# Kernel optimization log

Measured on AMD Instinct MI355X. Metric: run time of the kernel, lower is better.

## Reference

```python
import jax, jax.numpy as jnp
import numpy as np

B_, L_, H_ = 2, 2048, 2048          # batch, seq_len, hidden_size
I_, N_, NH, P_ = 4096, 128, 64, 64   # intermediate, ssm_state, num_heads, head_dim
K_, CH = 4, 256                      # conv kernel, chunk size
DT_MIN, DT_MAX = 0.0, 1e10


def setup_inputs() -> dict:
    key = jax.random.key(0)
    ks = jax.random.split(key, 8)
    conv_dim = I_ + 2 * N_
    proj_out = 2 * (I_ + N_) + NH
    return {
        "hidden_states": jax.random.normal(ks[0], (B_, L_, H_), jnp.float32),
        "W_in": jax.random.normal(ks[1], (proj_out, H_), jnp.float32) * 0.02,
        "conv_w": jax.random.normal(ks[2], (conv_dim, 1, K_), jnp.float32) * 0.2,
        "conv_b": jnp.zeros((conv_dim,), jnp.float32),
        "dt_bias": jax.random.uniform(ks[3], (NH,), jnp.float32),
        "A_log": jnp.log(jax.random.uniform(ks[4], (NH,), jnp.float32, 1.0, 16.0)),
        "D": jnp.ones((NH,), jnp.float32),
        "norm_w": jnp.ones((I_,), jnp.float32),
        "W_out": jax.random.normal(ks[5], (H_, I_), jnp.float32) * 0.02,
    }


def _segsum(x):
    # stable segment-sum: out[..., i, j] = sum_{k=j+1..i} x[..., k] for i>=j, else -inf
    T = x.shape[-1]
    xr = jnp.broadcast_to(x[..., None], x.shape + (T,))
    lower = jnp.tril(jnp.ones((T, T), bool), -1)
    s = jnp.cumsum(jnp.where(lower, xr, 0.0), axis=-2)
    return jnp.where(jnp.tril(jnp.ones((T, T), bool)), s, -jnp.inf)


def reference(hidden_states, W_in, conv_w, conv_b, dt_bias, A_log, D, norm_w, W_out):
    b, L, _ = hidden_states.shape
    proj = hidden_states @ W_in.T                       # (b, L, 2*(I+N)+H)
    z, xBC, dt = jnp.split(proj, [I_, 2 * I_ + 2 * N_], axis=-1)

    # depthwise causal conv1d + silu
    x_t = xBC.transpose(0, 2, 1)                        # (b, conv_dim, L)
    conv = jax.lax.conv_general_dilated(
        x_t, conv_w, (1,), [(K_ - 1, 0)],
        dimension_numbers=("NCH", "OIH", "NCH"), feature_group_count=I_ + 2 * N_)
    xBC = jax.nn.silu((conv + conv_b[None, :, None]).transpose(0, 2, 1))
    x, Bm, Cm = jnp.split(xBC, [I_, I_ + N_], axis=-1)  # (b,L,I) (b,L,N) (b,L,N)

    # ---- SSD naive (chunked state-space-duality scan) ----
    A = -jnp.exp(A_log.astype(jnp.float32))             # (h,)
    dt = jnp.clip(jax.nn.softplus(dt + dt_bias), DT_MIN, DT_MAX)  # (b,L,h)
    x4 = x.reshape(b, L, NH, P_)
    pad = (-L) % CH
    padf = lambda t: jnp.pad(t, [(0, 0), (0, pad)] + [(0, 0)] * (t.ndim - 2))
    D_res = D[None, None, :, None] * padf(x4)           # (b, Lp, h, p)
    xs = padf(x4 * dt[..., None])
    Ah = padf(A[None, None, :] * dt)                    # (b, Lp, h)
    Bc, Cc = padf(Bm), padf(Cm)
    c = (L + pad) // CH
    xs = xs.reshape(b, c, CH, NH, P_)                   # (b,c,l,h,p)
    Ah = Ah.reshape(b, c, CH, NH).transpose(0, 3, 1, 2) # (b,h,c,l)
    Bc = Bc.reshape(b, c, CH, N_)
    Cc = Cc.reshape(b, c, CH, N_)

    A_cs = jnp.cumsum(Ah, axis=-1)                      # (b,h,c,l)
    Lm = jnp.exp(_segsum(Ah))                           # (b,h,c,l,l)
    # intra-chunk (diagonal block) output; B/C shared across heads (n_groups=1)
    Y_diag = jnp.einsum("bcln,bcsn,bhcls,bcshp->bclhp", Cc, Bc, Lm, xs)

    decay_states = jnp.exp(A_cs[..., -1:] - A_cs)       # (b,h,c,l)
    states = jnp.einsum("bcln,bhcl,bclhp->bchpn", Bc, decay_states, xs)
    states = jnp.concatenate([jnp.zeros_like(states[:, :1]), states], axis=1)
    decay_chunk = jnp.exp(_segsum(jnp.pad(A_cs[..., -1], [(0, 0), (0, 0), (1, 0)])))
    new_states = jnp.einsum("bhzc,bchpn->bzhpn", decay_chunk, states)
    states = new_states[:, :-1]                         # (b,c,h,p,n)
    Y_off = jnp.einsum("bcln,bchpn,bhcl->bclhp", Cc, states, jnp.exp(A_cs))

    y = (Y_diag + Y_off).reshape(b, c * CH, NH, P_) + D_res
    y = y[:, :L].reshape(b, L, I_)

    # gated RMSNorm (normalize=True: multiply by silu(residual) before norm)
    yf = y.astype(jnp.float32) * jax.nn.silu(z.astype(jnp.float32))
    yf = yf * jax.lax.rsqrt(jnp.mean(yf * yf, -1, keepdims=True) + 1e-5) * norm_w
    return yf.astype(hidden_states.dtype) @ W_out.T
```

## Files before the change

### kernel.cpp

```cpp
#include <hip/hip_runtime.h>
#include <hip/hip_bf16.h>
#include <math.h>


#define B_SZ 2
#define L_SZ 2048
#define H_SZ 2048
#define I_SZ 4096
#define N_SZ 128
#define NH_SZ 64
#define P_SZ 64
#define CH_SZ 256
#define NC_SZ 8
#define PROJ_SZ 8512
#define CONV_SZ 4352
#define XOFF 4096
#define DTOFF 8448
#define BOFF 4096
#define COFF 4224

typedef __attribute__((ext_vector_type(8))) short short8_t;
typedef __attribute__((ext_vector_type(4))) float float4_t;

#define GLDS(gp, lp)                                                   \
  __builtin_amdgcn_global_load_lds(                                    \
      (const __attribute__((address_space(1))) void*)(gp),             \
      (__attribute__((address_space(3))) void*)(lp), 16, 0, 0)

__device__ __forceinline__ float bf2f(unsigned short u) {
  union { unsigned int i; float f; } v; v.i = ((unsigned int)u) << 16; return v.f;
}
__device__ __forceinline__ unsigned short f2bf(float f) {
  union { float f; unsigned int i; } v; v.f = f;
  unsigned int b = v.i + 0x7fffu + ((v.i >> 16) & 1u);
  return (unsigned short)(b >> 16);
}
__device__ __forceinline__ void unpack8(uint4 v, float* f) {
  f[0] = bf2f((unsigned short)(v.x & 0xffffu)); f[1] = bf2f((unsigned short)(v.x >> 16));
  f[2] = bf2f((unsigned short)(v.y & 0xffffu)); f[3] = bf2f((unsigned short)(v.y >> 16));
  f[4] = bf2f((unsigned short)(v.z & 0xffffu)); f[5] = bf2f((unsigned short)(v.z >> 16));
  f[6] = bf2f((unsigned short)(v.w & 0xffffu)); f[7] = bf2f((unsigned short)(v.w >> 16));
}
__device__ __forceinline__ float silu_f(float x) { return x / (1.f + expf(-x)); }

__device__ __forceinline__ float load1(const void* p, long long e, int fp32) {
  return fp32 ? ((const float*)p)[e] : bf2f(((const unsigned short*)p)[e]);
}
__device__ __forceinline__ void load4(const void* p, long long e, int fp32, float* f) {
  if (fp32) {
    float4 a = *(const float4*)((const float*)p + e);
    f[0] = a.x; f[1] = a.y; f[2] = a.z; f[3] = a.w;
  } else {
    uint2 v = *(const uint2*)((const unsigned short*)p + e);
    f[0] = bf2f((unsigned short)(v.x & 0xffffu)); f[1] = bf2f((unsigned short)(v.x >> 16));
    f[2] = bf2f((unsigned short)(v.y & 0xffffu)); f[3] = bf2f((unsigned short)(v.y >> 16));
  }
}
__device__ __forceinline__ void load8(const void* p, long long e, int fp32, float* f) {
  if (fp32) {
    float4 a = *(const float4*)((const float*)p + e);
    float4 b = *(const float4*)((const float*)p + e + 4);
    f[0] = a.x; f[1] = a.y; f[2] = a.z; f[3] = a.w;
    f[4] = b.x; f[5] = b.y; f[6] = b.z; f[7] = b.w;
  } else {
    uint4 v = *(const uint4*)((const unsigned short*)p + e);
    unpack8(v, f);
  }
}
__device__ __forceinline__ short8_t pack_bf8(const float* p) {
  float4 a = *(const float4*)p;
  float4 b = *(const float4*)(p + 4);
  short8_t r;
  r[0] = (short)f2bf(a.x); r[1] = (short)f2bf(a.y);
  r[2] = (short)f2bf(a.z); r[3] = (short)f2bf(a.w);
  r[4] = (short)f2bf(b.x); r[5] = (short)f2bf(b.y);
  r[6] = (short)f2bf(b.z); r[7] = (short)f2bf(b.w);
  return r;
}

__global__ void detect_k(const void* p0, const void* p1, const void* p2,
                         const void* p3, const void* p4, const void* p5,
                         const void* p6, const void* p7, const void* p8,
                         int n0, int n1, int n2, int n3, int n4, int n5,
                         int n6, int n7, int n8, int* flags) {
  __shared__ int pe, po;
  const void* ps[9] = {p0, p1, p2, p3, p4, p5, p6, p7, p8};
  int ns[9] = {n0, n1, n2, n3, n4, n5, n6, n7, n8};
  int t = threadIdx.x;
  for (int i = 0; i < 9; i++) {
    if (t == 0) { pe = 0; po = 0; }
    __syncthreads();
    int S = ns[i] < 256 ? ns[i] : 256;
    if (t < S) {
      unsigned short u = ((const unsigned short*)ps[i])[t];
      int ex = (u >> 7) & 0xFF;
      int plaus = ((u & 0x7FFFu) != 0) && (ex >= 0x70) && (ex <= 0x8F);
      if (plaus) { if (t & 1) atomicAdd(&po, 1); else atomicAdd(&pe, 1); }
    }
    __syncthreads();
    if (t == 0) flags[i] = (2 * pe < po) ? 1 : 0;
    __syncthreads();
  }
  if (t == 0) { flags[14] = 0; flags[15] = 0; }
}

__global__ __launch_bounds__(256)
void cvt_bf16_k(const void* __restrict__ src, unsigned short* __restrict__ dst,
                long long n8, const int* __restrict__ flags, int fi) {
  long long g = (long long)blockIdx.x * 256 + threadIdx.x;
  if (g >= n8) return;
  long long e = g * 8;
  if (flags[fi]) {
    const float* s = (const float*)src + e;
    float4 a = *(const float4*)s;
    float4 b = *(const float4*)(s + 4);
    unsigned short o[8] = {f2bf(a.x), f2bf(a.y), f2bf(a.z), f2bf(a.w),
                           f2bf(b.x), f2bf(b.y), f2bf(b.z), f2bf(b.w)};
    *(uint4*)(dst + e) = *(const uint4*)o;
  } else {
    *(uint4*)(dst + e) = *(const uint4*)((const unsigned short*)src + e);
  }
}

#define MFMA_ACC(d, a, b) \
  d = __builtin_amdgcn_mfma_f32_16x16x32_bf16(a, b, d, 0, 0, 0)
#define LDA_FR(buf, i, kk) \
  (*(const short8_t*)&As[(buf)*16384 + (wm*128 + (i)*16 + l16)*64 + \
                         (((((kk)<<2) + quad) ^ l7) << 3)])
#define LDB_FR(buf, j, kk) \
  (*(const short8_t*)&Bs[(buf)*16384 + (wn*64 + (j)*16 + l16)*64 + \
                         (((((kk)<<2) + quad) ^ l7) << 3)])
#define STAGE_A(h, tile, buf) do {                                          \
    GLDS(aSrc[h][0] + ((long long)(tile) << 6),                             \
         &As[(buf)*16384 + (h)*8192 + (wave*16)*64]);                       \
    GLDS(aSrc[h][1] + ((long long)(tile) << 6),                             \
         &As[(buf)*16384 + (h)*8192 + (wave*16 + 8)*64]);                   \
  } while (0)
#define STAGE_B(h, tile, buf) do {                                          \
    GLDS(bSrc[h][0] + ((long long)(tile) << 6),                             \
         &Bs[(buf)*16384 + (h)*8192 + (wave*16)*64]);                       \
    GLDS(bSrc[h][1] + ((long long)(tile) << 6),                             \
         &Bs[(buf)*16384 + (h)*8192 + (wave*16 + 8)*64]);                   \
  } while (0)

__global__ __launch_bounds__(512, 2)
void gemm_8ph_k(const unsigned short* __restrict__ A,
                const unsigned short* __restrict__ B,
                unsigned short* __restrict__ C,
                int N, int K, int lda, int ldb, int ldc, int gxTiles) {
  __shared__ alignas(16) unsigned short As[2 * 256 * 64];
  __shared__ alignas(16) unsigned short Bs[2 * 256 * 64];
  const int t = threadIdx.x;
  const int lane = t & 63;
  const int wave = t >> 6;
  const int quad = lane >> 4;
  const int l16 = lane & 15;
  const int l7 = lane & 7;
  const int l3 = lane >> 3;
  const int wm = wave >> 2;
  const int wn = wave & 3;

  int id = blockIdx.x;
  const int nwg = gridDim.x;
  int swz = id;
  if ((nwg & 7) == 0) swz = (id & 7) * (nwg >> 3) + (id >> 3);
  const int band = gxTiles << 2;
  const int by = (swz & 3) + ((swz / band) << 2);
  const int bx = (swz >> 2) % gxTiles;
  const int m0 = by << 8;
  const int n0 = bx << 8;
  const int NT = K >> 6;

  const int kperm = ((l7 ^ l3) << 3);
  const unsigned short* aSrc[2][2];
  const unsigned short* bSrc[2][2];
#pragma unroll
  for (int h = 0; h < 2; ++h)
#pragma unroll
    for (int c = 0; c < 2; ++c) {
      const int rloc = h * 128 + wave * 16 + c * 8 + l3;
      aSrc[h][c] = A + (long long)(m0 + rloc) * lda + kperm;
      int bn = n0 + rloc;
      if (bn > N - 1) bn = N - 1;
      bSrc[h][c] = B + (long long)bn * ldb + kperm;
    }

  float4_t acc[8][4];
#pragma unroll
  for (int i = 0; i < 8; ++i)
#pragma unroll
    for (int j = 0; j < 4; ++j) acc[i][j] = (float4_t){0.f, 0.f, 0.f, 0.f};

  STAGE_A(0, 0, 0); STAGE_A(1, 0, 0);
  STAGE_B(0, 0, 0); STAGE_B(1, 0, 0);
  STAGE_B(0, 1, 1); STAGE_B(1, 1, 1);
  asm volatile("s_waitcnt vmcnt(4)" ::: "memory");
  __builtin_amdgcn_s_barrier();

  short8_t af[4][2], bf[4][2];
  for (int tt = 0; tt < NT; ++tt) {
    const int rb = tt & 1, nb = rb ^ 1;
#pragma unroll
    for (int i = 0; i < 4; ++i) af[i][0] = LDA_FR(rb, i, 0);
#pragma unroll
    for (int j = 0; j < 4; ++j) bf[j][0] = LDB_FR(rb, j, 0);
    if (tt + 1 < NT) STAGE_A(0, tt + 1, nb);
    asm volatile("s_waitcnt lgkmcnt(4)" ::: "memory");
    __builtin_amdgcn_s_barrier();
    asm volatile("s_waitcnt lgkmcnt(0)" ::: "memory");
    __builtin_amdgcn_s_setprio(1);
#pragma unroll
    for (int i = 0; i < 4; ++i)
#pragma unroll
      for (int j = 0; j < 4; ++j) MFMA_ACC(acc[i][j], af[i][0], bf[j][0]);
    __builtin_amdgcn_s_setprio(0);
    __builtin_amdgcn_s_barrier();
#pragma unroll
    for (int i = 0; i < 4; ++i) af[i][1] = LDA_FR(rb, i, 1);
#pragma unroll
    for (int j = 0; j < 4; ++j) bf[j][1] = LDB_FR(rb, j, 1);
    if (tt + 1 < NT) STAGE_A(1, tt + 1, nb);
    asm volatile("s_waitcnt lgkmcnt(4)" ::: "memory");
    __builtin_amdgcn_s_barrier();
    asm volatile("s_waitcnt lgkmcnt(0)" ::: "memory");
    __builtin_amdgcn_s_setprio(1);
#pragma unroll
    for (int i = 0; i < 4; ++i)
#pragma unroll
      for (int j = 0; j < 4; ++j) MFMA_ACC(acc[i][j], af[i][1], bf[j][1]);
    __builtin_amdgcn_s_setprio(0);
    __builtin_amdgcn_s_barrier();
#pragma unroll
    for (int i = 0; i < 4; ++i) af[i][0] = LDA_FR(rb, 4 + i, 0);
    if (tt + 2 < NT) STAGE_B(0, tt + 2, rb);
    __builtin_amdgcn_s_barrier();
    asm volatile("s_waitcnt lgkmcnt(0)" ::: "memory");
    __builtin_amdgcn_s_setprio(1);
#pragma unroll
    for (int i = 0; i < 4; ++i)
#pragma unroll
      for (int j = 0; j < 4; ++j) MFMA_ACC(acc[4 + i][j], af[i][0], bf[j][0]);
    __builtin_amdgcn_s_setprio(0);
    __builtin_amdgcn_s_barrier();
#pragma unroll
    for (int i = 0; i < 4; ++i) af[i][1] = LDA_FR(rb, 4 + i, 1);
    if (tt + 2 < NT) STAGE_B(1, tt + 2, rb);
    __builtin_amdgcn_s_barrier();
    asm volatile("s_waitcnt lgkmcnt(0)" ::: "memory");
    __builtin_amdgcn_s_setprio(1);
#pragma unroll
    for (int i = 0; i < 4; ++i)
#pragma unroll
      for (int j = 0; j < 4; ++j) MFMA_ACC(acc[4 + i][j], af[i][1], bf[j][1]);
    __builtin_amdgcn_s_setprio(0);
    if (tt < NT - 2) asm volatile("s_waitcnt vmcnt(4)" ::: "memory");
    else             asm volatile("s_waitcnt vmcnt(0)" ::: "memory");
    __builtin_amdgcn_s_barrier();
  }

#pragma unroll
  for (int i = 0; i < 8; ++i) {
#pragma unroll
    for (int r = 0; r < 4; ++r) {
      const int m = m0 + wm * 128 + i * 16 + quad * 4 + r;
      const long long cb = (long long)m * ldc;
#pragma unroll
      for (int j = 0; j < 4; ++j) {
        const int n = n0 + wn * 64 + j * 16 + l16;
        if (n < N) C[cb + n] = f2bf(acc[i][j][r]);
      }
    }
  }
}

#define LDA2(buf, i, kk) \
  (*(const short8_t*)&As2[(buf)*8192 + (wm*64 + (i)*16 + l16)*64 + \
                          (((((kk)<<2) + quad) ^ l7) << 3)])
#define LDB2(buf, j, kk) \
  (*(const short8_t*)&Bs2[(buf)*8192 + (wn*64 + (j)*16 + l16)*64 + \
                          (((((kk)<<2) + quad) ^ l7) << 3)])

template <int OUT_MODE>
__global__ __launch_bounds__(256, 2)
void gemm_2ph_k(const unsigned short* __restrict__ A,
                const unsigned short* __restrict__ B,
                void* __restrict__ Cptr,
                int N, int K, int lda, int ldb, int ldc, int gxTiles,
                const int* __restrict__ flags, int fo) {
  __shared__ alignas(16) unsigned short As2[2 * 128 * 64];
  __shared__ alignas(16) unsigned short Bs2[2 * 128 * 64];
  const int t = threadIdx.x;
  const int lane = t & 63;
  const int wave = t >> 6;
  const int quad = lane >> 4;
  const int l16 = lane & 15;
  const int l7 = lane & 7;
  const int l3 = lane >> 3;
  const int wm = wave >> 1;
  const int wn = wave & 1;
  const int ofp = (OUT_MODE == 2) ? flags[fo] : 0;

  int id = blockIdx.x;
  const int nwg = gridDim.x;
  int swz = id;
  if ((nwg & 7) == 0) swz = (id & 7) * (nwg >> 3) + (id >> 3);
  const int band = gxTiles << 2;
  const int by = (swz & 3) + ((swz / band) << 2);
  const int bx = (swz >> 2) % gxTiles;
  const int m0 = by << 7;
  const int n0 = bx << 7;
  const int NT = K >> 6;

  const int kperm = ((l7 ^ l3) << 3);
  const unsigned short* aSrc[4];
  const unsigned short* bSrc[4];
#pragma unroll
  for (int c = 0; c < 4; ++c) {
    aSrc[c] = A + (long long)(m0 + wave * 32 + c * 8 + l3) * lda + kperm;
    int bn = n0 + wave * 32 + c * 8 + l3;
    if (bn > N - 1) bn = N - 1;
    bSrc[c] = B + (long long)bn * ldb + kperm;
  }

  float4_t acc[4][4];
#pragma unroll
  for (int i = 0; i < 4; ++i)
#pragma unroll
    for (int j = 0; j < 4; ++j) acc[i][j] = (float4_t){0.f, 0.f, 0.f, 0.f};

#pragma unroll
  for (int c = 0; c < 4; ++c) {
    GLDS(aSrc[c], &As2[(wave * 32 + c * 8) * 64]);
    GLDS(bSrc[c], &Bs2[(wave * 32 + c * 8) * 64]);
  }
  asm volatile("s_waitcnt vmcnt(0)" ::: "memory");
  __builtin_amdgcn_s_barrier();

  short8_t af[4], bfr[4];
  for (int tt = 0; tt < NT; ++tt) {
    const int rb = tt & 1, nb = rb ^ 1;
#pragma unroll
    for (int i = 0; i < 4; ++i) af[i] = LDA2(rb, i, 0);
#pragma unroll
    for (int j = 0; j < 4; ++j) bfr[j] = LDB2(rb, j, 0);
    if (tt + 1 < NT) {
      const long long ko = (long long)(tt + 1) << 6;
#pragma unroll
      for (int c = 0; c < 4; ++c) {
        GLDS(aSrc[c] + ko, &As2[nb * 8192 + (wave * 32 + c * 8) * 64]);
        GLDS(bSrc[c] + ko, &Bs2[nb * 8192 + (wave * 32 + c * 8) * 64]);
      }
    }
    __builtin_amdgcn_s_setprio(1);
#pragma unroll
    for (int i = 0; i < 4; ++i)
#pragma unroll
      for (int j = 0; j < 4; ++j) MFMA_ACC(acc[i][j], af[i], bfr[j]);
    __builtin_amdgcn_s_setprio(0);
#pragma unroll
    for (int i = 0; i < 4; ++i) af[i] = LDA2(rb, i, 1);
#pragma unroll
    for (int j = 0; j < 4; ++j) bfr[j] = LDB2(rb, j, 1);
    __builtin_amdgcn_s_setprio(1);
#pragma unroll
    for (int i = 0; i < 4; ++i)
#pragma unroll
      for (int j = 0; j < 4; ++j) MFMA_ACC(acc[i][j], af[i], bfr[j]);
    __builtin_amdgcn_s_setprio(0);
    asm volatile("s_waitcnt vmcnt(0)" ::: "memory");
    __builtin_amdgcn_s_barrier();
  }

#pragma unroll
  for (int i = 0; i < 4; ++i) {
#pragma unroll
    for (int r = 0; r < 4; ++r) {
      const int m = m0 + wm * 64 + i * 16 + quad * 4 + r;
      const long long cb = (long long)m * ldc;
#pragma unroll
      for (int j = 0; j < 4; ++j) {
        const int n = n0 + wn * 64 + j * 16 + l16;
        if (n < N) {
          float v = acc[i][j][r];
          if (ofp) ((float*)Cptr)[cb + n] = v;
          else     ((unsigned short*)Cptr)[cb + n] = f2bf(v);
        }
      }
    }
  }
}

__global__ __launch_bounds__(256)
void gemm_g_k(const unsigned short* __restrict__ convx,
              float* __restrict__ Gm) {
  const int t = threadIdx.x;
  const int lane = t & 63;
  const int wave = t >> 6;
  const int quad = lane >> 4;
  const int l16 = lane & 15;
  const int wm = wave >> 1, wn = wave & 1;
  const int m0 = blockIdx.y * 128 + wm * 64;
  const int n0 = blockIdx.x * 128 + wn * 64;
  const long long row0 = (long long)blockIdx.z * 256;

  float4_t acc[4][4];
#pragma unroll
  for (int i = 0; i < 4; ++i)
#pragma unroll
    for (int j = 0; j < 4; ++j) acc[i][j] = (float4_t){0.f, 0.f, 0.f, 0.f};

#pragma unroll
  for (int kt = 0; kt < 4; ++kt) {
    const int ko = kt * 32 + quad * 8;
    short8_t a[4], b[4];
#pragma unroll
    for (int i = 0; i < 4; ++i)
      a[i] = *(const short8_t*)&convx[(row0 + m0 + i * 16 + l16) * CONV_SZ + COFF + ko];
#pragma unroll
    for (int j = 0; j < 4; ++j)
      b[j] = *(const short8_t*)&convx[(row0 + n0 + j * 16 + l16) * CONV_SZ + BOFF + ko];
#pragma unroll
    for (int i = 0; i < 4; ++i)
#pragma unroll
      for (int j = 0; j < 4; ++j) MFMA_ACC(acc[i][j], a[i], b[j]);
  }
  float* Gb = Gm + (long long)blockIdx.z * 65536;
#pragma unroll
  for (int i = 0; i < 4; ++i)
#pragma unroll
    for (int r = 0; r < 4; ++r) {
      const int m = m0 + i * 16 + quad * 4 + r;
#pragma unroll
      for (int j = 0; j < 4; ++j)
        Gb[(long long)m * 256 + n0 + j * 16 + l16] = acc[i][j][r];
    }
}

__global__ __launch_bounds__(256)
void conv_silu_k(const unsigned short* __restrict__ proj,
                 const void* __restrict__ cw,
                 const void* __restrict__ cb,
                 unsigned short* __restrict__ convx,
                 const int* __restrict__ flags) {
  const int total = B_SZ * L_SZ * (CONV_SZ / 4);
  int g = blockIdx.x * 256 + threadIdx.x;
  if (g >= total) return;
  const int fw = flags[2], fb = flags[3];
  int c4 = g % (CONV_SZ / 4);
  int bl = g / (CONV_SZ / 4);
  int l = bl & (L_SZ - 1);
  int ch = c4 * 4;
  float w0[8], w1[8];
  load8(cw, (long long)ch * 4, fw, w0);
  load8(cw, (long long)ch * 4 + 8, fw, w1);
  float accv[4];
  load4(cb, ch, fb, accv);
  float acc0 = accv[0], acc1 = accv[1], acc2 = accv[2], acc3 = accv[3];
  const long long rb = (long long)(bl - l);
#pragma unroll
  for (int k = 0; k < 4; k++) {
    int ls = l - 3 + k;
    if (ls < 0) continue;
    uint2 xv = *(const uint2*)(proj + (rb + ls) * PROJ_SZ + XOFF + ch);
    float x0 = bf2f((unsigned short)(xv.x & 0xffffu));
    float x1 = bf2f((unsigned short)(xv.x >> 16));
    float x2 = bf2f((unsigned short)(xv.y & 0xffffu));
    float x3 = bf2f((unsigned short)(xv.y >> 16));
    acc0 = fmaf(x0, w0[k], acc0);
    acc1 = fmaf(x1, w0[4 + k], acc1);
    acc2 = fmaf(x2, w1[k], acc2);
    acc3 = fmaf(x3, w1[4 + k], acc3);
  }
  unsigned short o0 = f2bf(silu_f(acc0));
  unsigned short o1 = f2bf(silu_f(acc1));
  unsigned short o2 = f2bf(silu_f(acc2));
  unsigned short o3 = f2bf(silu_f(acc3));
  *(uint2*)(convx + (long long)bl * CONV_SZ + ch) =
      make_uint2((unsigned int)o0 | ((unsigned int)o1 << 16),
                 (unsigned int)o2 | ((unsigned int)o3 << 16));
}

__global__ __launch_bounds__(256)
void dt_prep_k(const unsigned short* __restrict__ proj,
               const void* __restrict__ dt_bias,
               float* __restrict__ dtv, const int* __restrict__ flags) {
  int g = blockIdx.x * 256 + threadIdx.x;
  int h = g & 63;
  long long bl = g >> 6;
  float v = bf2f(proj[bl * PROJ_SZ + DTOFF + h]) + load1(dt_bias, h, flags[4]);
  float sp = (v > 20.f) ? v : log1pf(expf(v));
  dtv[g] = sp;
}

__global__ __launch_bounds__(256)
void acs_scan_k(const float* __restrict__ dtv,
                const void* __restrict__ A_log,
                float* __restrict__ acs, const int* __restrict__ flags) {
  __shared__ float sd[256];
  int blk = blockIdx.x;
  int h = blk & 63;
  int bc = blk >> 6;
  int l = threadIdx.x;
  float Ah = -expf(load1(A_log, h, flags[5]));
  long long row = (long long)bc * CH_SZ + l;
  sd[l] = Ah * dtv[row * NH_SZ + h];
  for (int off = 1; off < 256; off <<= 1) {
    __syncthreads();
    float tv = (l >= off) ? sd[l - off] : 0.f;
    __syncthreads();
    sd[l] += tv;
  }
  acs[(long long)blk * CH_SZ + l] = sd[l];
}

__global__ __launch_bounds__(256)
void chunk_states_k(const unsigned short* __restrict__ convx,
                    const float* __restrict__ dtv,
                    const float* __restrict__ acs,
                    float* __restrict__ stc) {
  __shared__ float Bw[32][128];
  __shared__ float xw[32][64];
  int blk = blockIdx.x;
  int h = blk & 63;
  int bc = blk >> 6;
  int t = threadIdx.x;
  const int p0 = (t & 15) * 4, n0 = (t >> 4) * 8;
  const float* acsb = acs + (long long)blk * 256;
  const float alast = acsb[255];
  float acc[4][8];
#pragma unroll
  for (int i = 0; i < 4; i++)
#pragma unroll
    for (int j = 0; j < 8; j++) acc[i][j] = 0.f;
  const long long row0 = (long long)bc * 256;

  for (int lt0 = 0; lt0 < 256; lt0 += 32) {
    __syncthreads();
#pragma unroll
    for (int q = 0; q < 4; q++) {
      int idx4 = (t + 256 * q) * 4;
      int r = idx4 >> 7, n = idx4 & 127;
      uint2 v = *(const uint2*)(convx + (row0 + lt0 + r) * CONV_SZ + BOFF + n);
      Bw[r][n]     = bf2f((unsigned short)(v.x & 0xffffu));
      Bw[r][n + 1] = bf2f((unsigned short)(v.x >> 16));
      Bw[r][n + 2] = bf2f((unsigned short)(v.y & 0xffffu));
      Bw[r][n + 3] = bf2f((unsigned short)(v.y >> 16));
    }
#pragma unroll
    for (int q = 0; q < 2; q++) {
      int idx4 = (t + 256 * q) * 4;
      int r = idx4 >> 6, p = idx4 & 63;
      long long lg = row0 + lt0 + r;
      float sc = dtv[lg * NH_SZ + h] * expf(alast - acsb[lt0 + r]);
      uint2 v = *(const uint2*)(convx + lg * CONV_SZ + h * 64 + p);
      xw[r][p]     = bf2f((unsigned short)(v.x & 0xffffu)) * sc;
      xw[r][p + 1] = bf2f((unsigned short)(v.x >> 16)) * sc;
      xw[r][p + 2] = bf2f((unsigned short)(v.y & 0xffffu)) * sc;
      xw[r][p + 3] = bf2f((unsigned short)(v.y >> 16)) * sc;
    }
    __syncthreads();
#pragma unroll 4
    for (int lt = 0; lt < 32; lt++) {
      float4 xv = *(const float4*)&xw[lt][p0];
      float4 b0 = *(const float4*)&Bw[lt][n0];
      float4 b1 = *(const float4*)&Bw[lt][n0 + 4];
      float xa[4] = {xv.x, xv.y, xv.z, xv.w};
      float ba[8] = {b0.x, b0.y, b0.z, b0.w, b1.x, b1.y, b1.z, b1.w};
#pragma unroll
      for (int i = 0; i < 4; i++)
#pragma unroll
        for (int j = 0; j < 8; j++) acc[i][j] = fmaf(xa[i], ba[j], acc[i][j]);
    }
  }
  float* outb = stc + (long long)blk * 8192;
#pragma unroll
  for (int i = 0; i < 4; i++) {
    *(float4*)&outb[(p0 + i) * 128 + n0] =
        make_float4(acc[i][0], acc[i][1], acc[i][2], acc[i][3]);
    *(float4*)&outb[(p0 + i) * 128 + n0 + 4] =
        make_float4(acc[i][4], acc[i][5], acc[i][6], acc[i][7]);
  }
}

__global__ __launch_bounds__(256)
void recur_k(float* __restrict__ stc, const float* __restrict__ acs) {
  int blk = blockIdx.x;
  int b = blk >> 6, h = blk & 63;
  int t = threadIdx.x;
  float S[32];
#pragma unroll
  for (int j = 0; j < 32; j++) S[j] = 0.f;
  for (int z = 0; z < 8; z++) {
    long long bz = ((long long)b * 8 + z) * 64 + h;
    long long base = bz * 8192;
    float e = expf(acs[bz * 256 + 255]);
#pragma unroll
    for (int j = 0; j < 32; j++) {
      int idx = j * 256 + t;
      float cs = stc[base + idx];
      stc[base + idx] = S[j];
      S[j] = fmaf(e, S[j], cs);
    }
  }
}

__global__ __launch_bounds__(256)
void yoff_mfma_k(const unsigned short* __restrict__ convx,
                 const float* __restrict__ sti,
                 const float* __restrict__ acs,
                 const void* __restrict__ Dw,
                 float* __restrict__ y, const int* __restrict__ flags) {
  const int blk = blockIdx.x;
  const int h = blk & 63;
  const int bc = blk >> 6;
  const int t = threadIdx.x;
  const int lane = t & 63;
  const int wave = t >> 6;
  const int quad = lane >> 4;
  const int l16 = lane & 15;
  const int l0 = wave * 64;
  const long long row0 = (long long)bc * 256;
  const float* sib = sti + (long long)blk * 8192;
  const float* acsb = acs + (long long)blk * 256;
  const float Dh = load1(Dw, h, flags[6]);

  float4_t acc[4][4];
#pragma unroll
  for (int i = 0; i < 4; ++i)
#pragma unroll
    for (int j = 0; j < 4; ++j) acc[i][j] = (float4_t){0.f, 0.f, 0.f, 0.f};

#pragma unroll
  for (int kt = 0; kt < 4; ++kt) {
    const int ko = kt * 32 + quad * 8;
    short8_t a[4], b[4];
#pragma unroll
    for (int i = 0; i < 4; ++i)
      a[i] = *(const short8_t*)&convx[(row0 + l0 + i * 16 + l16) * CONV_SZ + COFF + ko];
#pragma unroll
    for (int j = 0; j < 4; ++j)
      b[j] = pack_bf8(sib + (j * 16 + l16) * 128 + ko);
#pragma unroll
    for (int i = 0; i < 4; ++i)
#pragma unroll
      for (int j = 0; j < 4; ++j) MFMA_ACC(acc[i][j], a[i], b[j]);
  }

#pragma unroll
  for (int i = 0; i < 4; ++i) {
#pragma unroll
    for (int r = 0; r < 4; ++r) {
      const int m = l0 + i * 16 + quad * 4 + r;
      const long long row = row0 + m;
      const float ex = expf(acsb[m]);
      const unsigned short* xr = convx + row * CONV_SZ + h * 64;
      float* yr = y + row * I_SZ + h * 64;
#pragma unroll
      for (int j = 0; j < 4; ++j) {
        const int p = j * 16 + l16;
        yr[p] = fmaf(ex, acc[i][j][r], Dh * bf2f(xr[p]));
      }
    }
  }
}

__global__ __launch_bounds__(256)
void ydiag_k(const unsigned short* __restrict__ convx,
             const float* __restrict__ dtv,
             const float* __restrict__ acs,
             const float* __restrict__ Gmat,
             float* __restrict__ y) {
  __shared__ float acs_s[256];
  __shared__ float xsT[64][68];
  __shared__ float Mt[64][66];
  int blk = blockIdx.x;
  int h = blk & 63;
  int bc = blk >> 6;
  int t = threadIdx.x;
  const int txp = t & 15, lq = t >> 4;
  acs_s[t] = acs[(long long)blk * 256 + t];
  const long long row0 = (long long)bc * 256;
  const float* Gb = Gmat + (long long)bc * 65536;
  for (int ltile = 0; ltile < 4; ltile++) {
    float acc[4][4] = {};
    for (int stile = 0; stile <= ltile; stile++) {
      __syncthreads();
#pragma unroll 4
      for (int q = 0; q < 16; q++) {
        int idx = t + 256 * q;
        int ss = idx >> 6, p = idx & 63;
        long long row = row0 + stile * 64 + ss;
        xsT[ss][p] = bf2f(convx[row * CONV_SZ + h * 64 + p]) * dtv[row * NH_SZ + h];
      }
#pragma unroll 4
      for (int q = 0; q < 16; q++) {
        int idx = t + 256 * q;
        int lr = idx >> 6, ss = idx & 63;
        int lg = ltile * 64 + lr, sg = stile * 64 + ss;
        float m = 0.f;
        if (sg <= lg) m = Gb[(long long)lg * 256 + sg] * expf(acs_s[lg] - acs_s[sg]);
        Mt[lr][ss] = m;
      }
      __syncthreads();
#pragma unroll 4
      for (int ss = 0; ss < 64; ss++) {
        float4 xv = *(const float4*)&xsT[ss][txp * 4];
        float m0 = Mt[lq * 4 + 0][ss];
        float m1 = Mt[lq * 4 + 1][ss];
        float m2 = Mt[lq * 4 + 2][ss];
        float m3 = Mt[lq * 4 + 3][ss];
        acc[0][0] = fmaf(m0, xv.x, acc[0][0]); acc[0][1] = fmaf(m0, xv.y, acc[0][1]);
        acc[0][2] = fmaf(m0, xv.z, acc[0][2]); acc[0][3] = fmaf(m0, xv.w, acc[0][3]);
        acc[1][0] = fmaf(m1, xv.x, acc[1][0]); acc[1][1] = fmaf(m1, xv.y, acc[1][1]);
        acc[1][2] = fmaf(m1, xv.z, acc[1][2]); acc[1][3] = fmaf(m1, xv.w, acc[1][3]);
        acc[2][0] = fmaf(m2, xv.x, acc[2][0]); acc[2][1] = fmaf(m2, xv.y, acc[2][1]);
        acc[2][2] = fmaf(m2, xv.z, acc[2][2]); acc[2][3] = fmaf(m2, xv.w, acc[2][3]);
        acc[3][0] = fmaf(m3, xv.x, acc[3][0]); acc[3][1] = fmaf(m3, xv.y, acc[3][1]);
        acc[3][2] = fmaf(m3, xv.z, acc[3][2]); acc[3][3] = fmaf(m3, xv.w, acc[3][3]);
      }
    }
#pragma unroll
    for (int i = 0; i < 4; i++) {
      long long row = row0 + ltile * 64 + lq * 4 + i;
      float* yp = &y[row * I_SZ + h * 64 + txp * 4];
      float4 cur = *(float4*)yp;
      cur.x += acc[i][0]; cur.y += acc[i][1]; cur.z += acc[i][2]; cur.w += acc[i][3];
      *(float4*)yp = cur;
    }
  }
}

__global__ __launch_bounds__(256)
void norm_k(const float* __restrict__ y,
            const unsigned short* __restrict__ proj,
            const void* __restrict__ nw,
            unsigned short* __restrict__ yfb, const int* __restrict__ flags) {
  __shared__ float red[4];
  __shared__ float sc_s;
  int row = blockIdx.x;
  int t = threadIdx.x;
  const int fn = flags[7];
  const float* yr = y + (long long)row * I_SZ;
  const unsigned short* zr = proj + (long long)row * PROJ_SZ;
  float g[16];
  float ss = 0.f;
#pragma unroll
  for (int q = 0; q < 4; q++) {
    int i0 = q * 1024 + t * 4;
    float4 yv = *(const float4*)&yr[i0];
    uint2 zv = *(const uint2*)&zr[i0];
    float z0 = bf2f((unsigned short)(zv.x & 0xffffu));
    float z1 = bf2f((unsigned short)(zv.x >> 16));
    float z2 = bf2f((unsigned short)(zv.y & 0xffffu));
    float z3 = bf2f((unsigned short)(zv.y >> 16));
    float g0 = yv.x * silu_f(z0), g1 = yv.y * silu_f(z1);
    float g2 = yv.z * silu_f(z2), g3 = yv.w * silu_f(z3);
    g[q * 4 + 0] = g0; g[q * 4 + 1] = g1; g[q * 4 + 2] = g2; g[q * 4 + 3] = g3;
    ss += g0 * g0 + g1 * g1 + g2 * g2 + g3 * g3;
  }
#pragma unroll
  for (int off = 32; off > 0; off >>= 1) ss += __shfl_down(ss, off, 64);
  if ((t & 63) == 0) red[t >> 6] = ss;
  __syncthreads();
  if (t == 0) sc_s = rsqrtf((red[0] + red[1] + red[2] + red[3]) * (1.f / 4096.f) + 1e-5f);
  __syncthreads();
  float sc = sc_s;
#pragma unroll
  for (int q = 0; q < 4; q++) {
    int i0 = q * 1024 + t * 4;
    float nv[4];
    load4(nw, i0, fn, nv);
    unsigned short o0 = f2bf(g[q * 4 + 0] * sc * nv[0]);
    unsigned short o1 = f2bf(g[q * 4 + 1] * sc * nv[1]);
    unsigned short o2 = f2bf(g[q * 4 + 2] * sc * nv[2]);
    unsigned short o3 = f2bf(g[q * 4 + 3] * sc * nv[3]);
    *(uint2*)&yfb[(long long)row * I_SZ + i0] =
        make_uint2((unsigned int)o0 | ((unsigned int)o1 << 16),
                   (unsigned int)o2 | ((unsigned int)o3 << 16));
  }
}

extern "C" void kernel_launch(void* const* d_in, const int* in_sizes, int n_in,
                              void* d_out, int out_size, void* d_ws, size_t ws_size,
                              hipStream_t stream) {
  const void* hs     = d_in[0];
  const void* W_in   = d_in[1];
  const void* conv_w = d_in[2];
  const void* conv_b = d_in[3];
  const void* dt_b   = d_in[4];
  const void* A_log  = d_in[5];
  const void* Dw     = d_in[6];
  const void* nw     = d_in[7];
  const void* W_out  = d_in[8];

  char* ws = (char*)d_ws;
  size_t off = 0;
  auto alloc = [&](size_t bytes) -> void* {
    void* p = ws + off;
    off += (bytes + 255) & ~(size_t)255;
    return p;
  };
  const long long ML = (long long)B_SZ * L_SZ;
  int* flags = (int*)alloc(64);
  unsigned short* proj  = (unsigned short*)alloc(ML * PROJ_SZ * 2);
  unsigned short* convx = (unsigned short*)alloc(ML * CONV_SZ * 2);
  float* dtv  = (float*)alloc(ML * NH_SZ * 4);
  float* acsb = (float*)alloc((long long)B_SZ * NC_SZ * NH_SZ * CH_SZ * 4);
  float* Gm   = (float*)alloc((long long)B_SZ * NC_SZ * CH_SZ * CH_SZ * 4);
  float* stc  = (float*)alloc((long long)B_SZ * NC_SZ * NH_SZ * P_SZ * N_SZ * 4);
  float* yb   = (float*)alloc(ML * I_SZ * 4);
  unsigned short* yfb = (unsigned short*)stc;
  unsigned short* hs_bf   = (unsigned short*)yb;
  unsigned short* Win_bf  = (unsigned short*)yb + 8388608;
  unsigned short* Wout_bf = (unsigned short*)yb;
  (void)n_in; (void)out_size;
  if (off > ws_size) return;

  dim3 blk(256);
  detect_k<<<1, blk, 0, stream>>>(hs, W_in, conv_w, conv_b, dt_b, A_log, Dw, nw, W_out,
                                  in_sizes[0], in_sizes[1], in_sizes[2], in_sizes[3],
                                  in_sizes[4], in_sizes[5], in_sizes[6], in_sizes[7],
                                  in_sizes[8], flags);
  cvt_bf16_k<<<dim3(4096), blk, 0, stream>>>(hs, hs_bf, 1048576LL, flags, 0);
  cvt_bf16_k<<<dim3(8512), blk, 0, stream>>>(W_in, Win_bf, 2179072LL, flags, 1);
  gemm_8ph_k<<<dim3(512), dim3(512), 0, stream>>>(
      hs_bf, Win_bf, proj, PROJ_SZ, H_SZ, H_SZ, H_SZ, PROJ_SZ, 32);
  gemm_2ph_k<0><<<dim3(96), blk, 0, stream>>>(
      hs_bf, Win_bf + 8192LL * 2048, proj + 8192, 320, H_SZ,
      H_SZ, H_SZ, PROJ_SZ, 3, flags, 15);
  conv_silu_k<<<dim3((B_SZ * L_SZ * (CONV_SZ / 4) + 255) / 256), blk, 0, stream>>>(
      proj, conv_w, conv_b, convx, flags);
  dt_prep_k<<<dim3((unsigned)(ML * NH_SZ / 256)), blk, 0, stream>>>(proj, dt_b, dtv, flags);
  acs_scan_k<<<dim3(B_SZ * NC_SZ * NH_SZ), blk, 0, stream>>>(dtv, A_log, acsb, flags);
  gemm_g_k<<<dim3(2, 2, 16), blk, 0, stream>>>(convx, Gm);
  chunk_states_k<<<dim3(1024), blk, 0, stream>>>(convx, dtv, acsb, stc);
  recur_k<<<dim3(B_SZ * NH_SZ), blk, 0, stream>>>(stc, acsb);
  yoff_mfma_k<<<dim3(1024), blk, 0, stream>>>(convx, stc, acsb, Dw, yb, flags);
  ydiag_k<<<dim3(1024), blk, 0, stream>>>(convx, dtv, acsb, Gm, yb);
  norm_k<<<dim3((unsigned)ML), blk, 0, stream>>>(yb, proj, nw, yfb, flags);
  cvt_bf16_k<<<dim3(4096), blk, 0, stream>>>(W_out, Wout_bf, 1048576LL, flags, 8);
  gemm_2ph_k<2><<<dim3(512), blk, 0, stream>>>(
      yfb, Wout_bf, d_out, H_SZ, I_SZ, I_SZ, I_SZ, H_SZ, 16,
      flags, 0);
}
```

Before: 677.8 us.

## Rewrite intra-chunk Y_diag kernel to use bf16 MFMA with whole-chunk LDS staging

The scalar-FMA ydiag kernel, which tiled the causal 256x256 mask times x*dt in 64-wide chunks with repeated syncs, is replaced by an MFMA version. The whole chunk of dt-scaled x is staged once in LDS as transposed bf16. Each wave owns 64 output rows and builds the masked decay matrix fragments directly in registers before issuing MFMA ops over only the causal s-range. This removes the per-tile barriers and the scalar FMA loops, at the cost of bf16 rounding of the mask and x, and uneven work across waves.

```diff
diff --git a/kernel.cpp b/kernel.cpp
--- a/kernel.cpp
+++ b/kernel.cpp
@@ -665,67 +665,87 @@
 }
 
 __global__ __launch_bounds__(256)
-void ydiag_k(const unsigned short* __restrict__ convx,
-             const float* __restrict__ dtv,
-             const float* __restrict__ acs,
-             const float* __restrict__ Gmat,
-             float* __restrict__ y) {
+void ydiag_mfma_k(const unsigned short* __restrict__ convx,
+                  const float* __restrict__ dtv,
+                  const float* __restrict__ acs,
+                  const float* __restrict__ Gmat,
+                  float* __restrict__ y) {
+  __shared__ alignas(16) unsigned short xsT[64 * 264];
   __shared__ float acs_s[256];
-  __shared__ float xsT[64][68];
-  __shared__ float Mt[64][66];
-  int blk = blockIdx.x;
-  int h = blk & 63;
-  int bc = blk >> 6;
-  int t = threadIdx.x;
-  const int txp = t & 15, lq = t >> 4;
-  acs_s[t] = acs[(long long)blk * 256 + t];
+  const int blk = blockIdx.x;
+  const int h = blk & 63;
+  const int bc = blk >> 6;
+  const int t = threadIdx.x;
+  const int lane = t & 63;
+  const int wave = t >> 6;
+  const int quad = lane >> 4;
+  const int l16 = lane & 15;
   const long long row0 = (long long)bc * 256;
   const float* Gb = Gmat + (long long)bc * 65536;
-  for (int ltile = 0; ltile < 4; ltile++) {
-    float acc[4][4] = {};
-    for (int stile = 0; stile <= ltile; stile++) {
-      __syncthreads();
+
+  acs_s[t] = acs[(long long)blk * 256 + t];
 #pragma unroll 4
-      for (int q = 0; q < 16; q++) {
-        int idx = t + 256 * q;
-        int ss = idx >> 6, p = idx & 63;
-        long long row = row0 + stile * 64 + ss;
-        xsT[ss][p] = bf2f(convx[row * CONV_SZ + h * 64 + p]) * dtv[row * NH_SZ + h];
+  for (int q = 0; q < 32; ++q) {
+    int idx = t + 256 * q;
+    int s2 = idx >> 6, p = idx & 63;
+    int s = s2 * 2;
+    long long r0 = row0 + s;
+    float d0 = dtv[r0 * NH_SZ + h];
+    float d1 = dtv[(r0 + 1) * NH_SZ + h];
+    float v0 = bf2f(convx[r0 * CONV_SZ + h * 64 + p]) * d0;
+    float v1 = bf2f(convx[(r0 + 1) * CONV_SZ + h * 64 + p]) * d1;
+    *(unsigned int*)&xsT[p * 264 + s] =
+        (unsigned int)f2bf(v0) | ((unsigned int)f2bf(v1) << 16);
+  }
+  __syncthreads();
+
+  float4_t acc[4][4];
+#pragma unroll
+  for (int i = 0; i < 4; ++i)
+#pragma unroll
+    for (int j = 0; j < 4; ++j) acc[i][j] = (float4_t){0.f, 0.f, 0.f, 0.f};
+
+  const int l0 = wave * 64;
+  const int nst = 2 * wave + 2;
+  for (int st = 0; st < nst; ++st) {
+    const int sb = st * 32 + quad * 8;
+    short8_t a[4], b[4];
+#pragma unroll
+    for (int i = 0; i < 4; ++i) {
+      const int lg = l0 + i * 16 + l16;
+      const float al = acs_s[lg];
+      const float* gr = Gb + (long long)lg * 256 + sb;
+      short8_t m;
+#pragma unroll
+      for (int e = 0; e < 8; ++e) {
+        const int sg = sb + e;
+        float v = 0.f;
+        if (sg <= lg)
+          v = gr[e] * exp2f((al - acs_s[sg]) * 1.4426950408889634f);
+        m[e] = (short)f2bf(v);
       }
-#pragma unroll 4
-      for (int q = 0; q < 16; q++) {
-        int idx = t + 256 * q;
-        int lr = idx >> 6, ss = idx & 63;
-        int lg = ltile * 64 + lr, sg = stile * 64 + ss;
-        float m = 0.f;
-        if (sg <= lg) m = Gb[(long long)lg * 256 + sg] * expf(acs_s[lg] - acs_s[sg]);
-        Mt[lr][ss] = m;
+      a[i] = m;
+    }
+#pragma unroll
+    for (int j = 0; j < 4; ++j)
+      b[j] = *(const short8_t*)&xsT[(j * 16 + l16) * 264 + sb];
+#pragma unroll
+    for (int i = 0; i < 4; ++i)
+#pragma unroll
+      for (int j = 0; j < 4; ++j) MFMA_ACC(acc[i][j], a[i], b[j]);
+  }
+
+#pragma unroll
+  for (int i = 0; i < 4; ++i) {
+#pragma unroll
+    for (int r = 0; r < 4; ++r) {
+      const int m = l0 + i * 16 + quad * 4 + r;
+      float* yr = y + (row0 + m) * I_SZ + h * 64;
+#pragma unroll
+      for (int j = 0; j < 4; ++j) {
+        const int p = j * 16 + l16;
+        yr[p] += acc[i][j][r];
       }
-      __syncthreads();
-#pragma unroll 4
-      for (int ss = 0; ss < 64; ss++) {
-        float4 xv = *(const float4*)&xsT[ss][txp * 4];
-        float m0 = Mt[lq * 4 + 0][ss];
-        float m1 = Mt[lq * 4 + 1][ss];
-        float m2 = Mt[lq * 4 + 2][ss];
-        float m3 = Mt[lq * 4 + 3][ss];
-        acc[0][0] = fmaf(m0, xv.x, acc[0][0]); acc[0][1] = fmaf(m0, xv.y, acc[0][1]);
-        acc[0][2] = fmaf(m0, xv.z, acc[0][2]); acc[0][3] = fmaf(m0, xv.w, acc[0][3]);
-        acc[1][0] = fmaf(m1, xv.x, acc[1][0]); acc[1][1] = fmaf(m1, xv.y, acc[1][1]);
-        acc[1][2] = fmaf(m1, xv.z, acc[1][2]); acc[1][3] = fmaf(m1, xv.w, acc[1][3]);
-        acc[2][0] = fmaf(m2, xv.x, acc[2][0]); acc[2][1] = fmaf(m2, xv.y, acc[2][1]);
-        acc[2][2] = fmaf(m2, xv.z, acc[2][2]); acc[2][3] = fmaf(m2, xv.w, acc[2][3]);
-        acc[3][0] = fmaf(m3, xv.x, acc[3][0]); acc[3][1] = fmaf(m3, xv.y, acc[3][1]);
-        acc[3][2] = fmaf(m3, xv.z, acc[3][2]); acc[3][3] = fmaf(m3, xv.w, acc[3][3]);
-      }
-    }
-#pragma unroll
-    for (int i = 0; i < 4; i++) {
-      long long row = row0 + ltile * 64 + lq * 4 + i;
-      float* yp = &y[row * I_SZ + h * 64 + txp * 4];
-      float4 cur = *(float4*)yp;
-      cur.x += acc[i][0]; cur.y += acc[i][1]; cur.z += acc[i][2]; cur.w += acc[i][3];
-      *(float4*)yp = cur;
     }
   }
 }
@@ -836,7 +856,7 @@
   chunk_states_k<<<dim3(1024), blk, 0, stream>>>(convx, dtv, acsb, stc);
   recur_k<<<dim3(B_SZ * NH_SZ), blk, 0, stream>>>(stc, acsb);
   yoff_mfma_k<<<dim3(1024), blk, 0, stream>>>(convx, stc, acsb, Dw, yb, flags);
-  ydiag_k<<<dim3(1024), blk, 0, stream>>>(convx, dtv, acsb, Gm, yb);
+  ydiag_mfma_k<<<dim3(1024), blk, 0, stream>>>(convx, dtv, acsb, Gm, yb);
   norm_k<<<dim3((unsigned)ML), blk, 0, stream>>>(yb, proj, nw, yfb, flags);
   cvt_bf16_k<<<dim3(4096), blk, 0, stream>>>(W_out, Wout_bf, 1048576LL, flags, 8);
   gemm_2ph_k<2><<<dim3(512), blk, 0, stream>>>(
```

New measurement: 663.3 us. 2.1% less time.
